# Kernel optimization log

Measured on AMD Instinct MI355X. Metric: run time of the kernel, lower is better.

Reference implementation:

```python
import jax, jax.numpy as jnp
import numpy as np

B, N, D = 4, 2048, 1024
G = 256          # group_size
QK = 128         # query_key_dim
H = 2048         # hidden_dim = int(dim * expansion_factor)
LN_EPS = 1e-5


def setup_inputs() -> dict:
    key = jax.random.key(0)
    ks = jax.random.split(key, 6)
    s = 0.02
    return {
        "x": jax.random.normal(ks[0], (B, N, D), jnp.float32),
        "ln_g": jnp.ones((D,), jnp.float32),
        "ln_b": jnp.zeros((D,), jnp.float32),
        "W_hidden": jax.random.normal(ks[1], (D, 2 * H), jnp.float32) * s,
        "b_hidden": jnp.zeros((2 * H,), jnp.float32),
        "W_qk": jax.random.normal(ks[2], (D, QK), jnp.float32) * s,
        "b_qk": jnp.zeros((QK,), jnp.float32),
        "os_gamma": jnp.ones((4, QK), jnp.float32) + jax.random.normal(ks[3], (4, QK), jnp.float32) * 0.02,
        "os_beta": jnp.zeros((4, QK), jnp.float32),
        "W_out": jax.random.normal(ks[4], (H, D), jnp.float32) * s,
        "b_out": jnp.zeros((D,), jnp.float32),
    }


def _rope(x):
    # x: [b, n, d]; rotary over the sequence dim, matching FLASH.rope(x, dim=1)
    n, d = x.shape[-2], x.shape[-1]
    half = d // 2
    pos = jnp.arange(n, dtype=jnp.float32)
    # freq_seq = -arange(half)/half; inv_freq = 10000 ** (-freq_seq)
    inv_freq = jnp.power(10000.0, jnp.arange(half, dtype=jnp.float32) / half)
    sinusoid = pos[:, None] * inv_freq[None, :]            # [n, half]
    sin, cos = jnp.sin(sinusoid), jnp.cos(sinusoid)
    x1, x2 = jnp.split(x, 2, axis=-1)
    return jnp.concatenate([x1 * cos - x2 * sin, x2 * cos + x1 * sin], axis=-1)


def reference(x, ln_g, ln_b, W_hidden, b_hidden, W_qk, b_qk,
              os_gamma, os_beta, W_out, b_out):
    b, n, d = x.shape
    g = G
    # LayerNorm (biased variance, as torch)
    mu = jnp.mean(x, -1, keepdims=True)
    var = jnp.mean(jnp.square(x - mu), -1, keepdims=True)
    normed = (x - mu) / jnp.sqrt(var + LN_EPS) * ln_g + ln_b

    h = jax.nn.silu(normed @ W_hidden + b_hidden)          # [b, n, 2H]
    v, gate = jnp.split(h, 2, axis=-1)                     # [b, n, H] each
    qk = jax.nn.silu(normed @ W_qk + b_qk)                 # [b, n, QK]

    # OffsetScale: 4 heads -> quad_q, lin_q, quad_k, lin_k
    qk4 = qk[..., None, :] * os_gamma + os_beta            # [b, n, 4, QK]
    quad_q, lin_q, quad_k, lin_k = (_rope(qk4[..., i, :]) for i in range(4))

    pad = (-n) % g
    if pad:
        padf = lambda t: jnp.pad(t, ((0, 0), (0, pad), (0, 0)))
        quad_q, quad_k, lin_q, lin_k, v_p = map(padf, (quad_q, quad_k, lin_q, lin_k, v))
    else:
        v_p = v
    grp = lambda t: t.reshape(b, -1, g, t.shape[-1])       # b (g n) d -> b g n d
    quad_q, quad_k, lin_q, lin_k, vg = map(grp, (quad_q, quad_k, lin_q, lin_k, v_p))

    # group-local quadratic attention with ReLU^2
    sim = jnp.einsum('bgid,bgjd->bgij', quad_q, quad_k) / g
    attn = jnp.square(jax.nn.relu(sim))
    quad_out = jnp.einsum('bgij,bgje->bgie', attn, vg)

    # linear global attention (reduced over groups), divided by full seq len n
    lin_kv = jnp.einsum('bgnd,bgne->bde', lin_k, vg) / n
    lin_out = jnp.einsum('bgnd,bde->bgne', lin_q, lin_kv)

    out = (quad_out + lin_out).reshape(b, -1, vg.shape[-1])[:, :n]
    out = gate * out
    return out @ W_out + b_out + x
```

## Files before the change

kernel.cpp:

```cpp
#include <hip/hip_runtime.h>
#include <stdint.h>

typedef __attribute__((ext_vector_type(8))) short bf16x8_t;
typedef __attribute__((ext_vector_type(4))) float f32x4_t;

#define DI __device__ __forceinline__
#define SBAR() asm volatile("s_barrier" ::: "memory")
#define VMW(n) asm volatile("s_waitcnt vmcnt(" #n ")" ::: "memory")

DI unsigned short f2b(float f) {
  union { float f; unsigned int u; } c; c.f = f;
  unsigned int u = c.u + 0x7FFFu + ((c.u >> 16) & 1u);
  return (unsigned short)(u >> 16);
}
DI unsigned int pack2(float lo, float hi) {
  return (unsigned int)f2b(lo) | ((unsigned int)f2b(hi) << 16);
}
DI float b2f(unsigned short h) {
  union { unsigned int u; float f; } c; c.u = ((unsigned int)h) << 16;
  return c.f;
}
DI float silu_f(float z) { return z / (1.0f + __expf(-z)); }

DI void load_lds16(const unsigned short* g, unsigned short* l) {
  __builtin_amdgcn_global_load_lds(
      (const __attribute__((address_space(1))) unsigned int*)g,
      (__attribute__((address_space(3))) unsigned int*)l,
      16, 0, 0);
}

struct PrepP {
  const float *Wh, *Wo, *Wqk, *x, *g, *b;
  unsigned short *WT, *WoT, *normed;
};

__global__ __launch_bounds__(256) void prep_kernel(PrepP p) {
  const int blk = blockIdx.x;
  const int tx = threadIdx.x & 31, ty = threadIdx.x >> 5;
  if (blk < 6272) {
    const float* in; unsigned short* out; int R, C, gx;
    if (blk < 4096)      { in = p.Wh;  out = p.WT;                 R = 1024; C = 4096; gx = blk; }
    else if (blk < 6144) { in = p.Wo;  out = p.WoT;                R = 2048; C = 1024; gx = blk - 4096; }
    else                 { in = p.Wqk; out = p.WT + 4096 * 1024;   R = 1024; C = 128;  gx = blk - 6144; }
    const int xTiles = C >> 5;
    const int c0 = (gx % xTiles) * 32, r0 = (gx / xTiles) * 32;
    __shared__ float tile[32][33];
#pragma unroll
    for (int i = 0; i < 4; ++i)
      tile[ty + 8 * i][tx] = in[(long)(r0 + ty + 8 * i) * C + c0 + tx];
    __syncthreads();
#pragma unroll
    for (int i = 0; i < 4; ++i)
      out[(long)(c0 + ty + 8 * i) * R + r0 + tx] = f2b(tile[tx][ty + 8 * i]);
  } else {
    const int row = blk - 6272, tid = threadIdx.x;
    __shared__ float red[8];
    float4 v = ((const float4*)(p.x + (long)row * 1024))[tid];
    float s = v.x + v.y + v.z + v.w;
    float ss = v.x * v.x + v.y * v.y + v.z * v.z + v.w * v.w;
    for (int o = 32; o > 0; o >>= 1) { s += __shfl_down(s, o); ss += __shfl_down(ss, o); }
    const int wave = tid >> 6, lane = tid & 63;
    if (lane == 0) { red[wave * 2] = s; red[wave * 2 + 1] = ss; }
    __syncthreads();
    if (tid == 0) {
      float S = red[0] + red[2] + red[4] + red[6];
      float SS = red[1] + red[3] + red[5] + red[7];
      float mu = S * (1.0f / 1024.0f);
      float var = SS * (1.0f / 1024.0f) - mu * mu;
      red[0] = mu; red[1] = rsqrtf(var + 1e-5f);
    }
    __syncthreads();
    const float mu = red[0], rstd = red[1];
    float4 gg = ((const float4*)p.g)[tid];
    float4 bb = ((const float4*)p.b)[tid];
    ushort4 o;
    o.x = f2b((v.x - mu) * rstd * gg.x + bb.x);
    o.y = f2b((v.y - mu) * rstd * gg.y + bb.y);
    o.z = f2b((v.z - mu) * rstd * gg.z + bb.z);
    o.w = f2b((v.w - mu) * rstd * gg.w + bb.w);
    ((ushort4*)(p.normed + (long)row * 1024))[tid] = o;
  }
}

__global__ __launch_bounds__(256) void reduce_cvt(
    const unsigned short* __restrict__ part, unsigned short* __restrict__ out) {
  const int idx = blockIdx.x * 256 + threadIdx.x;
  const int b = idx >> 16, i = idx & 65535;
  float4 s = make_float4(0.f, 0.f, 0.f, 0.f);
#pragma unroll
  for (int sl = 0; sl < 8; ++sl) {
    ushort4 v = ((const ushort4*)part)[(long)(b * 8 + sl) * 65536 + i];
    s.x += b2f(v.x); s.y += b2f(v.y); s.z += b2f(v.z); s.w += b2f(v.w);
  }
  ushort4 o;
  o.x = f2b(s.x); o.y = f2b(s.y); o.z = f2b(s.z); o.w = f2b(s.w);
  ((ushort4*)out)[(long)b * 65536 + i] = o;
}

struct G8P {
  const unsigned short* A;
  const unsigned short* B;
  const float* bias;
  const float* bias2;
  const float* gamma;
  const float* beta;
  unsigned short* vTout;
  unsigned short* gateOut;
  unsigned short* qqO;
  unsigned short* lqO;
  unsigned short* qkhO;
  unsigned short* lkTO;
};

__global__ __launch_bounds__(512, 4) void gemm8p(G8P p) {
  extern __shared__ unsigned char lds[];
  const int tid  = threadIdx.x;
  const int lane = tid & 63;
  const int wave = tid >> 6;
  const bool qk = blockIdx.x < 32;
  int bx, by;
  if (qk) { bx = blockIdx.x; by = 32; }
  else    { const int vg = blockIdx.x - 32; bx = vg >> 5; by = vg & 31; }
  const int wm = (wave & 1) * 128;
  const int wn = (wave >> 1) * 32;
  const int lm = lane & 15;
  const int kb = lane >> 4;

  const int rA  = tid >> 2;
  const int kby = ((tid & 3) << 4) ^ (((rA >> 1) & 3) << 4);
  const unsigned short* gA0 = p.A + (long)(bx * 256 + rA) * 1024 + (kby >> 1);
  const unsigned short* gA1 = gA0 + 128 * 1024;
  const int brow = qk ? 4096 : by * 128;
  const unsigned short* gB0 = p.B + (long)(brow + rA) * 1024 + (kby >> 1);

  const int fxor = (kb << 4) ^ (((lm >> 1) & 3) << 4);

  f32x4_t acc[8][2];
#pragma unroll
  for (int i = 0; i < 8; ++i)
#pragma unroll
    for (int j = 0; j < 2; ++j) acc[i][j] = (f32x4_t){0.f, 0.f, 0.f, 0.f};

  auto stageA = [&](int t) {
    unsigned short* l = (unsigned short*)(lds + (t % 3) * 24576 + wave * 1024);
    load_lds16(gA0 + t * 32, l);
    load_lds16(gA1 + t * 32, (unsigned short*)((unsigned char*)l + 8192));
  };
  auto stageB = [&](int t) {
    unsigned short* l = (unsigned short*)(lds + (t % 3) * 24576 + 16384 + wave * 1024);
    load_lds16(gB0 + t * 32, l);
  };

#pragma unroll
  for (int u = 0; u < 2; ++u) { stageA(u); stageB(u); }
  VMW(3);
  SBAR();

  constexpr int NT = 16;
#pragma unroll 1
  for (int t = 0; t < NT; ++t) {
    const unsigned char* slot = lds + (t % 3) * 24576;
    bf16x8_t bF[2], aF[4];
#pragma unroll
    for (int j = 0; j < 2; ++j)
      bF[j] = *(const bf16x8_t*)(slot + 16384 + (wn + j * 16 + lm) * 64 + fxor);
#pragma unroll
    for (int i = 0; i < 4; ++i)
      aF[i] = *(const bf16x8_t*)(slot + (wm + i * 16 + lm) * 64 + fxor);
    if (t <= NT - 3) stageA(t + 2);
    __builtin_amdgcn_s_setprio(1);
#pragma unroll
    for (int i = 0; i < 4; ++i)
#pragma unroll
      for (int j = 0; j < 2; ++j)
        acc[i][j] = __builtin_amdgcn_mfma_f32_16x16x32_bf16(aF[i], bF[j], acc[i][j], 0, 0, 0);
    __builtin_amdgcn_s_setprio(0);
#pragma unroll
    for (int i = 0; i < 4; ++i)
      aF[i] = *(const bf16x8_t*)(slot + (wm + 64 + i * 16 + lm) * 64 + fxor);
    if (t <= NT - 3) stageB(t + 2);
    __builtin_amdgcn_s_setprio(1);
#pragma unroll
    for (int i = 0; i < 4; ++i)
#pragma unroll
      for (int j = 0; j < 2; ++j)
        acc[i + 4][j] = __builtin_amdgcn_mfma_f32_16x16x32_bf16(aF[i], bF[j], acc[i + 4][j], 0, 0, 0);
    __builtin_amdgcn_s_setprio(0);
    if (t <= NT - 3)      { VMW(3); }
    else if (t == NT - 2) { VMW(0); }
    SBAR();
  }

  if (qk) {
    unsigned short* q16 = (unsigned short*)lds;
#pragma unroll
    for (int i = 0; i < 8; ++i) {
      const int rloc = wm + i * 16 + (lane >> 4) * 4;
#pragma unroll
      for (int j = 0; j < 2; ++j) {
        const int cl = wn + j * 16 + lm;
        const float bb = p.bias2[cl];
#pragma unroll
        for (int r = 0; r < 4; ++r)
          q16[(rloc + r) * 136 + cl] = f2b(silu_f(acc[i][j][r] + bb));
      }
    }
    __syncthreads();
    const int j = tid & 63;
    const int rq = tid >> 6;
    const float freq = powf(10000.0f, (float)j * (1.0f / 64.0f));
    float ga[4], gb[4], ea[4], eb[4];
#pragma unroll
    for (int h = 0; h < 4; ++h) {
      ga[h] = p.gamma[h * 128 + j];  gb[h] = p.gamma[h * 128 + 64 + j];
      ea[h] = p.beta[h * 128 + j];   eb[h] = p.beta[h * 128 + 64 + j];
    }
    unsigned short* outs[3] = {p.qqO, p.lqO, p.qkhO};
    for (int rr = 0; rr < 32; ++rr) {
      const int row = rr * 8 + rq;
      const float x1 = b2f(q16[row * 136 + j]);
      const float x2 = b2f(q16[row * 136 + 64 + j]);
      const int tok = bx * 256 + row;
      const int pos = tok & 2047, bidx = tok >> 11;
      const float ang = (float)pos * freq;
      const float sn = sinf(ang), cs = cosf(ang);
#pragma unroll
      for (int h = 0; h < 3; ++h) {
        const float y1 = x1 * ga[h] + ea[h], y2 = x2 * gb[h] + eb[h];
        outs[h][(long)tok * 128 + j] = f2b(y1 * cs - y2 * sn);
        outs[h][(long)tok * 128 + 64 + j] = f2b(y2 * cs + y1 * sn);
      }
      const float y1 = x1 * ga[3] + ea[3], y2 = x2 * gb[3] + eb[3];
      p.lkTO[((long)bidx * 128 + j) * 2048 + pos] = f2b(y1 * cs - y2 * sn);
      p.lkTO[((long)bidx * 128 + 64 + j) * 2048 + pos] = f2b(y2 * cs + y1 * sn);
    }
  } else if (by < 16) {
    unsigned int* Cx = (unsigned int*)lds;
#pragma unroll
    for (int i = 0; i < 8; ++i) {
      const int c0 = (wm + i * 16) / 2 + (lane >> 4) * 2;
#pragma unroll
      for (int j = 0; j < 2; ++j) {
        const int e = wn + j * 16 + lm;
        const float bb = p.bias[by * 128 + e];
        const float s0 = silu_f(acc[i][j][0] + bb);
        const float s1 = silu_f(acc[i][j][1] + bb);
        const float s2 = silu_f(acc[i][j][2] + bb);
        const float s3 = silu_f(acc[i][j][3] + bb);
        const int x = (e & 7) << 2;
        Cx[e * 128 + (c0 ^ x)]     = pack2(s0, s1);
        Cx[e * 128 + (c0 ^ x) + 1] = pack2(s2, s3);
      }
    }
    __syncthreads();
    const int bq = bx >> 3, nloc0 = (bx & 7) * 256, e0g = by * 128;
    unsigned short* dstBase = p.vTout + ((long)(bq * 2048 + e0g)) * 2048 + nloc0;
#pragma unroll
    for (int rep = 0; rep < 8; ++rep) {
      const int flat = rep * 512 + tid;
      const int e = flat >> 5, q = flat & 31;
      uint4 val = *(const uint4*)(Cx + e * 128 + ((q ^ (e & 7)) << 2));
      *(uint4*)(dstBase + (long)e * 2048 + q * 8) = val;
    }
  } else {
#pragma unroll
    for (int i = 0; i < 8; ++i) {
      const int row0 = bx * 256 + wm + i * 16 + (lane >> 4) * 4;
#pragma unroll
      for (int j = 0; j < 2; ++j) {
        const int colg = (by - 16) * 128 + wn + j * 16 + lm;
        const float bb = p.bias[2048 + colg];
#pragma unroll
        for (int r = 0; r < 4; ++r)
          p.gateOut[(long)(row0 + r) * 2048 + colg] =
              f2b(silu_f(acc[i][j][r] + bb));
      }
    }
  }
}

struct GQLP {
  const unsigned short* attn;
  const unsigned short* vT;
  const unsigned short* lq;
  const unsigned short* lkvT;
  const unsigned short* gateIn;
  unsigned short* outU;
};

__global__ __launch_bounds__(512, 4) void gemmQL(GQLP p) {
  extern __shared__ unsigned char lds[];
  const int tid  = threadIdx.x;
  const int lane = tid & 63;
  const int wave = tid >> 6;
  const int z  = blockIdx.x >> 4;
  const int by = blockIdx.x & 15;
  const int b = z >> 3, g = z & 7;
  const int wm = (wave & 1) * 128;
  const int wn = (wave >> 1) * 32;
  const int lm = lane & 15;
  const int kb = lane >> 4;

  const int rA  = tid >> 2;
  const int kby = ((tid & 3) << 4) ^ (((rA >> 1) & 3) << 4);
  const int swz = kby >> 1;
  const unsigned short* a1 = p.attn + (long)z * 65536 + rA * 256 + swz;
  const unsigned short* a2 = p.lq + ((long)z * 256 + rA) * 128 + swz;
  const unsigned short* b1 = p.vT + (long)b * 4194304 + (long)(by * 128 + rA) * 2048 + g * 256 + swz;
  const unsigned short* b2 = p.lkvT + (long)b * 262144 + (by * 128 + rA) * 128 + swz;
  const int fxor = (kb << 4) ^ (((lm >> 1) & 3) << 4);

  f32x4_t acc[8][2];
#pragma unroll
  for (int i = 0; i < 8; ++i)
#pragma unroll
    for (int j = 0; j < 2; ++j) acc[i][j] = (f32x4_t){0.f, 0.f, 0.f, 0.f};

  auto stageA = [&](int tt) {
    unsigned char* base = lds + (tt % 3) * 24576;
    unsigned short* l  = (unsigned short*)(base + wave * 1024);
    unsigned short* lh = (unsigned short*)(base + wave * 1024 + 8192);
    if (tt < 8) { load_lds16(a1 + tt * 32, l); load_lds16(a1 + 128 * 256 + tt * 32, lh); }
    else { const int k2 = (tt - 8) * 32;
           load_lds16(a2 + k2, l); load_lds16(a2 + 128 * 128 + k2, lh); }
  };
  auto stageB = [&](int tt) {
    unsigned short* l = (unsigned short*)(lds + (tt % 3) * 24576 + 16384 + wave * 1024);
    if (tt < 8) load_lds16(b1 + tt * 32, l);
    else        load_lds16(b2 + (tt - 8) * 32, l);
  };

#pragma unroll
  for (int u = 0; u < 2; ++u) { stageA(u); stageB(u); }
  VMW(3);
  SBAR();

  constexpr int NT = 12;
#pragma unroll 1
  for (int t = 0; t < NT; ++t) {
    const unsigned char* slot = lds + (t % 3) * 24576;
    bf16x8_t bF[2], aF[4];
#pragma unroll
    for (int j = 0; j < 2; ++j)
      bF[j] = *(const bf16x8_t*)(slot + 16384 + (wn + j * 16 + lm) * 64 + fxor);
#pragma unroll
    for (int i = 0; i < 4; ++i)
      aF[i] = *(const bf16x8_t*)(slot + (wm + i * 16 + lm) * 64 + fxor);
    if (t <= NT - 3) stageA(t + 2);
    __builtin_amdgcn_s_setprio(1);
#pragma unroll
    for (int i = 0; i < 4; ++i)
#pragma unroll
      for (int j = 0; j < 2; ++j)
        acc[i][j] = __builtin_amdgcn_mfma_f32_16x16x32_bf16(aF[i], bF[j], acc[i][j], 0, 0, 0);
    __builtin_amdgcn_s_setprio(0);
#pragma unroll
    for (int i = 0; i < 4; ++i)
      aF[i] = *(const bf16x8_t*)(slot + (wm + 64 + i * 16 + lm) * 64 + fxor);
    if (t <= NT - 3) stageB(t + 2);
    __builtin_amdgcn_s_setprio(1);
#pragma unroll
    for (int i = 0; i < 4; ++i)
#pragma unroll
      for (int j = 0; j < 2; ++j)
        acc[i + 4][j] = __builtin_amdgcn_mfma_f32_16x16x32_bf16(aF[i], bF[j], acc[i + 4][j], 0, 0, 0);
    __builtin_amdgcn_s_setprio(0);
    if (t <= NT - 3)      { VMW(3); }
    else if (t == NT - 2) { VMW(0); }
    SBAR();
  }

#pragma unroll
  for (int i = 0; i < 8; ++i) {
    const int row0 = z * 256 + wm + i * 16 + (lane >> 4) * 4;
#pragma unroll
    for (int j = 0; j < 2; ++j) {
      const int col = by * 128 + wn + j * 16 + lm;
#pragma unroll
      for (int r = 0; r < 4; ++r) {
        const long idx = (long)(row0 + r) * 2048 + col;
        p.outU[idx] = f2b(b2f(p.gateIn[idx]) * acc[i][j][r]);
      }
    }
  }
}

struct GWoP {
  const unsigned short* A;
  const unsigned short* B;
  const float* bias;
  const float* xres;
  float* outF;
};

__global__ __launch_bounds__(512, 2) void gemmWo(GWoP p) {
  extern __shared__ unsigned char lds[];
  const int tid  = threadIdx.x;
  const int lane = tid & 63;
  const int wave = tid >> 6;
  const int bx = blockIdx.x >> 3;
  const int by = blockIdx.x & 7;
  const int wm = (wave & 1) * 128;
  const int wn = (wave >> 1) * 32;
  const int lm = lane & 15;
  const int kb = lane >> 4;

  const int rA  = tid >> 2;
  const int kby = ((tid & 3) << 4) ^ (((rA >> 1) & 3) << 4);
  const unsigned short* gA0 = p.A + (long)(bx * 256 + rA) * 2048 + (kby >> 1);
  const unsigned short* gA1 = gA0 + 128 * 2048;
  const unsigned short* gB0 = p.B + (long)(by * 128 + rA) * 2048 + (kby >> 1);
  const int fxor = (kb << 4) ^ (((lm >> 1) & 3) << 4);

  f32x4_t acc[8][2];
#pragma unroll
  for (int i = 0; i < 8; ++i)
#pragma unroll
    for (int j = 0; j < 2; ++j) acc[i][j] = (f32x4_t){0.f, 0.f, 0.f, 0.f};

  auto stageA = [&](int t) {
    unsigned short* l = (unsigned short*)(lds + (t & 3) * 24576 + wave * 1024);
    load_lds16(gA0 + t * 32, l);
    load_lds16(gA1 + t * 32, (unsigned short*)((unsigned char*)l + 8192));
  };
  auto stageB = [&](int t) {
    unsigned short* l = (unsigned short*)(lds + (t & 3) * 24576 + 16384 + wave * 1024);
    load_lds16(gB0 + t * 32, l);
  };

#pragma unroll
  for (int u = 0; u < 3; ++u) { stageA(u); stageB(u); }
  VMW(6);
  SBAR();

  constexpr int NT = 64;
#pragma unroll 1
  for (int t = 0; t < NT; ++t) {
    const unsigned char* slot = lds + (t & 3) * 24576;
    bf16x8_t bF[2], aF[4];
#pragma unroll
    for (int j = 0; j < 2; ++j)
      bF[j] = *(const bf16x8_t*)(slot + 16384 + (wn + j * 16 + lm) * 64 + fxor);
#pragma unroll
    for (int i = 0; i < 4; ++i)
      aF[i] = *(const bf16x8_t*)(slot + (wm + i * 16 + lm) * 64 + fxor);
    if (t <= NT - 4) stageA(t + 3);
    __builtin_amdgcn_s_setprio(1);
#pragma unroll
    for (int i = 0; i < 4; ++i)
#pragma unroll
      for (int j = 0; j < 2; ++j)
        acc[i][j] = __builtin_amdgcn_mfma_f32_16x16x32_bf16(aF[i], bF[j], acc[i][j], 0, 0, 0);
    __builtin_amdgcn_s_setprio(0);
#pragma unroll
    for (int i = 0; i < 4; ++i)
      aF[i] = *(const bf16x8_t*)(slot + (wm + 64 + i * 16 + lm) * 64 + fxor);
    if (t <= NT - 4) stageB(t + 3);
    __builtin_amdgcn_s_setprio(1);
#pragma unroll
    for (int i = 0; i < 4; ++i)
#pragma unroll
      for (int j = 0; j < 2; ++j)
        acc[i + 4][j] = __builtin_amdgcn_mfma_f32_16x16x32_bf16(aF[i], bF[j], acc[i + 4][j], 0, 0, 0);
    __builtin_amdgcn_s_setprio(0);
    if (t <= NT - 4)      { VMW(6); }
    else if (t == NT - 3) { VMW(3); }
    else if (t == NT - 2) { VMW(0); }
    SBAR();
  }

#pragma unroll
  for (int i = 0; i < 8; ++i) {
    const int row0 = bx * 256 + wm + i * 16 + (lane >> 4) * 4;
#pragma unroll
    for (int j = 0; j < 2; ++j) {
      const int col = by * 128 + wn + j * 16 + lm;
      const float bb = p.bias[col];
#pragma unroll
      for (int r = 0; r < 4; ++r) {
        const long idx = (long)(row0 + r) * 1024 + col;
        p.outF[idx] = acc[i][j][r] + bb + p.xres[idx];
      }
    }
  }
}

enum { EPI_ARELU, EPI_PART };

struct GemmP {
  const unsigned short* A;
  const unsigned short* B;
  int K, lda, ldb, ldc, mPerZ;
  long aZ, bZ;
  float scale;
  unsigned short* outU;
};

template <int EPI>
__global__ __launch_bounds__(256, 2) void gemm_bt(GemmP p) {
  __shared__ __align__(16) unsigned char smem[16384];
  unsigned short* As = (unsigned short*)smem;
  unsigned short* Bs = (unsigned short*)(smem + 8192);

  const int tid = threadIdx.x;
  const int lane = tid & 63;
  const int wave = tid >> 6;
  const int bx = blockIdx.x;
  const int by = blockIdx.y;
  const int z = blockIdx.z;

  unsigned short* lA = As + wave * 32 * 32;
  unsigned short* lB = Bs + wave * 32 * 32;
  const int wm = (wave & 1) * 64;
  const int wn = (wave >> 1) * 64;
  const int lm = lane & 15;
  const int kb = lane >> 4;
  const int rowSel = (wave * 32 + (lane >> 2));
  const int colSel = (lane & 3) * 8;

  f32x4_t acc[4][4];
#pragma unroll
  for (int i = 0; i < 4; ++i)
#pragma unroll
    for (int j = 0; j < 4; ++j) acc[i][j] = (f32x4_t){0.f, 0.f, 0.f, 0.f};

  const unsigned short* Ag;
  const unsigned short* Bg;
  if constexpr (EPI == EPI_PART) {
    const int b = z >> 3, s = z & 7;
    Ag = p.A + (long)b * p.aZ + s * 256 + (long)(bx * 128 + rowSel) * p.lda + colSel;
    Bg = p.B + (long)b * p.bZ + s * 256 + (long)(by * 128 + rowSel) * p.ldb + colSel;
  } else {
    Ag = p.A + (long)z * p.aZ + (long)(bx * 128 + rowSel) * p.lda + colSel;
    Bg = p.B + (long)z * p.bZ + (long)(by * 128 + rowSel) * p.ldb + colSel;
  }
  const int a16 = 16 * p.lda, b16 = 16 * p.ldb;
  for (int kt = 0; kt < (p.K >> 5); ++kt) {
    load_lds16(Ag, lA);
    load_lds16(Ag + a16, lA + 512);
    load_lds16(Bg, lB);
    load_lds16(Bg + b16, lB + 512);
    Ag += 32; Bg += 32;
    __syncthreads();
    bf16x8_t aF[4], bF[4];
#pragma unroll
    for (int i = 0; i < 4; ++i)
      aF[i] = *(const bf16x8_t*)(As + (wm + i * 16 + lm) * 32 + kb * 8);
#pragma unroll
    for (int j = 0; j < 4; ++j)
      bF[j] = *(const bf16x8_t*)(Bs + (wn + j * 16 + lm) * 32 + kb * 8);
#pragma unroll
    for (int i = 0; i < 4; ++i)
#pragma unroll
      for (int j = 0; j < 4; ++j)
        acc[i][j] = __builtin_amdgcn_mfma_f32_16x16x32_bf16(aF[i], bF[j], acc[i][j], 0, 0, 0);
    __syncthreads();
  }

#pragma unroll
  for (int i = 0; i < 4; ++i) {
    const int row0 = bx * 128 + wm + i * 16 + (lane >> 4) * 4;
    long rowg0;
    if constexpr (EPI == EPI_PART) rowg0 = row0;
    else rowg0 = (long)z * p.mPerZ + row0;
#pragma unroll
    for (int j = 0; j < 4; ++j) {
      const int col = by * 128 + wn + j * 16 + lm;
      if constexpr (EPI == EPI_ARELU) {
#pragma unroll
        for (int r = 0; r < 4; ++r) {
          float s = acc[i][j][r] * p.scale;
          s = s > 0.f ? s : 0.f;
          p.outU[(rowg0 + r) * (long)p.ldc + col] = f2b(s * s);
        }
      } else {
        unsigned short* slab = p.outU + (long)z * 262144;
#pragma unroll
        for (int r = 0; r < 4; ++r)
          slab[(rowg0 + r) * (long)p.ldc + col] = f2b(acc[i][j][r] * p.scale);
      }
    }
  }
}

extern "C" void kernel_launch(void* const* d_in, const int* in_sizes, int n_in,
                              void* d_out, int out_size, void* d_ws, size_t ws_size,
                              hipStream_t stream) {
  const float* x        = (const float*)d_in[0];
  const float* ln_g     = (const float*)d_in[1];
  const float* ln_b     = (const float*)d_in[2];
  const float* W_hidden = (const float*)d_in[3];
  const float* b_hidden = (const float*)d_in[4];
  const float* W_qk     = (const float*)d_in[5];
  const float* b_qk     = (const float*)d_in[6];
  const float* os_gamma = (const float*)d_in[7];
  const float* os_beta  = (const float*)d_in[8];
  const float* W_out    = (const float*)d_in[9];
  const float* b_out    = (const float*)d_in[10];
  float* out = (float*)d_out;

  char* w = (char*)d_ws;
  auto ws = [&](size_t bytes) { char* p = w; w += bytes; return (unsigned short*)p; };
  unsigned short* WT     = ws(8650752);
  unsigned short* WoT    = ws(4194304);
  unsigned short* normed = ws(16777216);
  unsigned short* vT     = ws(33554432);
  unsigned short* gate   = ws(33554432);
  unsigned short* qq     = ws(2097152);
  unsigned short* qkh    = ws(2097152);
  unsigned short* lq     = ws(2097152);
  unsigned short* lkT    = ws(2097152);
  unsigned short* attn   = ws(4194304);
  unsigned short* lkvP   = ws(16777216);
  unsigned short* lkvT   = ws(2097152);
  unsigned short* A3     = ws(33554432);

  static bool s_attr = false;
  if (!s_attr) {
    hipFuncSetAttribute((const void*)gemm8p,
                        hipFuncAttributeMaxDynamicSharedMemorySize, 73728);
    hipFuncSetAttribute((const void*)gemmQL,
                        hipFuncAttributeMaxDynamicSharedMemorySize, 73728);
    hipFuncSetAttribute((const void*)gemmWo,
                        hipFuncAttributeMaxDynamicSharedMemorySize, 98304);
    s_attr = true;
  }

  {
    PrepP p{W_hidden, W_out, W_qk, x, ln_g, ln_b, WT, WoT, normed};
    prep_kernel<<<14464, 256, 0, stream>>>(p);
  }
  {
    G8P p{normed, WT, b_hidden, b_qk, os_gamma, os_beta,
          vT, gate, qq, lq, qkh, lkT};
    gemm8p<<<dim3(1056, 1, 1), 512, 73728, stream>>>(p);
  }
  {
    GemmP p{}; p.A = qq; p.B = qkh; p.K = 128; p.lda = 128; p.ldb = 128;
    p.ldc = 256; p.mPerZ = 256; p.aZ = 32768; p.bZ = 32768;
    p.scale = 1.f / 256.f; p.outU = attn;
    gemm_bt<EPI_ARELU><<<dim3(2, 2, 32), 256, 0, stream>>>(p);
  }
  {
    GemmP p{}; p.A = vT; p.B = lkT; p.K = 256; p.lda = 2048; p.ldb = 2048;
    p.ldc = 128; p.aZ = 4194304; p.bZ = 262144;
    p.scale = 1.f / 2048.f; p.outU = lkvP;
    gemm_bt<EPI_PART><<<dim3(16, 1, 32), 256, 0, stream>>>(p);
  }
  reduce_cvt<<<1024, 256, 0, stream>>>(lkvP, lkvT);
  {
    GQLP p{attn, vT, lq, lkvT, gate, A3};
    gemmQL<<<dim3(512, 1, 1), 512, 73728, stream>>>(p);
  }
  {
    GWoP p{A3, WoT, b_out, x, out};
    gemmWo<<<dim3(256, 1, 1), 512, 98304, stream>>>(p);
  }
}
```

Before: 297.1 us.

## Shrink output GEMM tile to 128x128 and reuse pipelined kernel for lin_kv partials

The output projection GEMM moves from 256x128 tiles with a 4-stage buffer to 128x128 tiles with a 3-stage buffer and 48KB LDS. That doubles the grid to 512 blocks and allows up to 4 blocks per CU, giving better occupancy and CU coverage. The same templated kernel replaces the simple synchronous gemm_bt for the lin_kv partial products, so that step gets the swizzled, async-pipelined loads. In exchange, the smaller tiles mean more global traffic per FLOP and a shallower prefetch depth.

```diff
diff --git a/kernel.cpp b/kernel.cpp
--- a/kernel.cpp
+++ b/kernel.cpp
@@ -385,66 +385,74 @@
   }
 }
 
-struct GWoP {
+struct G1P {
   const unsigned short* A;
   const unsigned short* B;
   const float* bias;
   const float* xres;
   float* outF;
+  unsigned short* outU;
 };
 
-__global__ __launch_bounds__(512, 2) void gemmWo(GWoP p) {
+template <int EPI>
+__global__ __launch_bounds__(512, 4) void gemm128(G1P p) {
   extern __shared__ unsigned char lds[];
   const int tid  = threadIdx.x;
   const int lane = tid & 63;
   const int wave = tid >> 6;
-  const int bx = blockIdx.x >> 3;
-  const int by = blockIdx.x & 7;
-  const int wm = (wave & 1) * 128;
+  const int wm = (wave & 1) * 64;
   const int wn = (wave >> 1) * 32;
   const int lm = lane & 15;
   const int kb = lane >> 4;
-
   const int rA  = tid >> 2;
   const int kby = ((tid & 3) << 4) ^ (((rA >> 1) & 3) << 4);
-  const unsigned short* gA0 = p.A + (long)(bx * 256 + rA) * 2048 + (kby >> 1);
-  const unsigned short* gA1 = gA0 + 128 * 2048;
-  const unsigned short* gB0 = p.B + (long)(by * 128 + rA) * 2048 + (kby >> 1);
+  const int swz = kby >> 1;
   const int fxor = (kb << 4) ^ (((lm >> 1) & 3) << 4);
 
-  f32x4_t acc[8][2];
-#pragma unroll
-  for (int i = 0; i < 8; ++i)
+  int bx, byz;
+  const unsigned short* gA;
+  const unsigned short* gB;
+  if constexpr (EPI == 0) {
+    bx  = blockIdx.x >> 3;
+    byz = blockIdx.x & 7;
+    gA = p.A + (long)(bx * 128 + rA) * 2048 + swz;
+    gB = p.B + (long)(byz * 128 + rA) * 2048 + swz;
+  } else {
+    byz = blockIdx.x >> 4;
+    bx  = blockIdx.x & 15;
+    const int b = byz >> 3, s = byz & 7;
+    gA = p.A + (long)b * 4194304 + (long)(bx * 128 + rA) * 2048 + s * 256 + swz;
+    gB = p.B + (long)b * 262144 + rA * 2048 + s * 256 + swz;
+  }
+
+  f32x4_t acc[4][2];
+#pragma unroll
+  for (int i = 0; i < 4; ++i)
 #pragma unroll
     for (int j = 0; j < 2; ++j) acc[i][j] = (f32x4_t){0.f, 0.f, 0.f, 0.f};
 
-  auto stageA = [&](int t) {
-    unsigned short* l = (unsigned short*)(lds + (t & 3) * 24576 + wave * 1024);
-    load_lds16(gA0 + t * 32, l);
-    load_lds16(gA1 + t * 32, (unsigned short*)((unsigned char*)l + 8192));
+  auto stage = [&](int t) {
+    unsigned char* base = lds + (t % 3) * 16384;
+    load_lds16(gA + t * 32, (unsigned short*)(base + wave * 1024));
+    load_lds16(gB + t * 32, (unsigned short*)(base + 8192 + wave * 1024));
   };
-  auto stageB = [&](int t) {
-    unsigned short* l = (unsigned short*)(lds + (t & 3) * 24576 + 16384 + wave * 1024);
-    load_lds16(gB0 + t * 32, l);
-  };
-
-#pragma unroll
-  for (int u = 0; u < 3; ++u) { stageA(u); stageB(u); }
-  VMW(6);
+
+  stage(0); stage(1);
+  VMW(2);
   SBAR();
 
-  constexpr int NT = 64;
+  constexpr int NT = (EPI == 0) ? 64 : 8;
 #pragma unroll 1
   for (int t = 0; t < NT; ++t) {
-    const unsigned char* slot = lds + (t & 3) * 24576;
+    const unsigned char* slot = lds + (t % 3) * 16384;
     bf16x8_t bF[2], aF[4];
 #pragma unroll
     for (int j = 0; j < 2; ++j)
-      bF[j] = *(const bf16x8_t*)(slot + 16384 + (wn + j * 16 + lm) * 64 + fxor);
+      bF[j] = *(const bf16x8_t*)(slot + 8192 + (wn + j * 16 + lm) * 64 + fxor);
 #pragma unroll
     for (int i = 0; i < 4; ++i)
       aF[i] = *(const bf16x8_t*)(slot + (wm + i * 16 + lm) * 64 + fxor);
-    if (t <= NT - 4) stageA(t + 3);
+    if (t <= NT - 3) stage(t + 2);
     __builtin_amdgcn_s_setprio(1);
 #pragma unroll
     for (int i = 0; i < 4; ++i)
@@ -452,40 +460,41 @@
       for (int j = 0; j < 2; ++j)
         acc[i][j] = __builtin_amdgcn_mfma_f32_16x16x32_bf16(aF[i], bF[j], acc[i][j], 0, 0, 0);
     __builtin_amdgcn_s_setprio(0);
-#pragma unroll
-    for (int i = 0; i < 4; ++i)
-      aF[i] = *(const bf16x8_t*)(slot + (wm + 64 + i * 16 + lm) * 64 + fxor);
-    if (t <= NT - 4) stageB(t + 3);
-    __builtin_amdgcn_s_setprio(1);
-#pragma unroll
-    for (int i = 0; i < 4; ++i)
-#pragma unroll
-      for (int j = 0; j < 2; ++j)
-        acc[i + 4][j] = __builtin_amdgcn_mfma_f32_16x16x32_bf16(aF[i], bF[j], acc[i + 4][j], 0, 0, 0);
-    __builtin_amdgcn_s_setprio(0);
-    if (t <= NT - 4)      { VMW(6); }
-    else if (t == NT - 3) { VMW(3); }
+    if (t <= NT - 3)      { VMW(2); }
     else if (t == NT - 2) { VMW(0); }
     SBAR();
   }
 
-#pragma unroll
-  for (int i = 0; i < 8; ++i) {
-    const int row0 = bx * 256 + wm + i * 16 + (lane >> 4) * 4;
-#pragma unroll
-    for (int j = 0; j < 2; ++j) {
-      const int col = by * 128 + wn + j * 16 + lm;
-      const float bb = p.bias[col];
-#pragma unroll
-      for (int r = 0; r < 4; ++r) {
-        const long idx = (long)(row0 + r) * 1024 + col;
-        p.outF[idx] = acc[i][j][r] + bb + p.xres[idx];
-      }
-    }
-  }
-}
-
-enum { EPI_ARELU, EPI_PART };
+  if constexpr (EPI == 0) {
+#pragma unroll
+    for (int i = 0; i < 4; ++i) {
+      const int row0 = bx * 128 + wm + i * 16 + (lane >> 4) * 4;
+#pragma unroll
+      for (int j = 0; j < 2; ++j) {
+        const int col = byz * 128 + wn + j * 16 + lm;
+        const float bb = p.bias[col];
+#pragma unroll
+        for (int r = 0; r < 4; ++r) {
+          const long idx = (long)(row0 + r) * 1024 + col;
+          p.outF[idx] = acc[i][j][r] + bb + p.xres[idx];
+        }
+      }
+    }
+  } else {
+    unsigned short* slab = p.outU + (long)byz * 262144;
+#pragma unroll
+    for (int i = 0; i < 4; ++i) {
+      const int row0 = bx * 128 + wm + i * 16 + (lane >> 4) * 4;
+#pragma unroll
+      for (int j = 0; j < 2; ++j) {
+        const int col = wn + j * 16 + lm;
+#pragma unroll
+        for (int r = 0; r < 4; ++r)
+          slab[(row0 + r) * 128 + col] = f2b(acc[i][j][r] * (1.0f / 2048.0f));
+      }
+    }
+  }
+}
 
 struct GemmP {
   const unsigned short* A;
@@ -496,8 +505,7 @@
   unsigned short* outU;
 };
 
-template <int EPI>
-__global__ __launch_bounds__(256, 2) void gemm_bt(GemmP p) {
+__global__ __launch_bounds__(256, 2) void gemm_arelu(GemmP p) {
   __shared__ __align__(16) unsigned char smem[16384];
   unsigned short* As = (unsigned short*)smem;
   unsigned short* Bs = (unsigned short*)(smem + 8192);
@@ -524,16 +532,8 @@
 #pragma unroll
     for (int j = 0; j < 4; ++j) acc[i][j] = (f32x4_t){0.f, 0.f, 0.f, 0.f};
 
-  const unsigned short* Ag;
-  const unsigned short* Bg;
-  if constexpr (EPI == EPI_PART) {
-    const int b = z >> 3, s = z & 7;
-    Ag = p.A + (long)b * p.aZ + s * 256 + (long)(bx * 128 + rowSel) * p.lda + colSel;
-    Bg = p.B + (long)b * p.bZ + s * 256 + (long)(by * 128 + rowSel) * p.ldb + colSel;
-  } else {
-    Ag = p.A + (long)z * p.aZ + (long)(bx * 128 + rowSel) * p.lda + colSel;
-    Bg = p.B + (long)z * p.bZ + (long)(by * 128 + rowSel) * p.ldb + colSel;
-  }
+  const unsigned short* Ag = p.A + (long)z * p.aZ + (long)(bx * 128 + rowSel) * p.lda + colSel;
+  const unsigned short* Bg = p.B + (long)z * p.bZ + (long)(by * 128 + rowSel) * p.ldb + colSel;
   const int a16 = 16 * p.lda, b16 = 16 * p.ldb;
   for (int kt = 0; kt < (p.K >> 5); ++kt) {
     load_lds16(Ag, lA);
@@ -559,25 +559,15 @@
 
 #pragma unroll
   for (int i = 0; i < 4; ++i) {
-    const int row0 = bx * 128 + wm + i * 16 + (lane >> 4) * 4;
-    long rowg0;
-    if constexpr (EPI == EPI_PART) rowg0 = row0;
-    else rowg0 = (long)z * p.mPerZ + row0;
+    const long rowg0 = (long)z * p.mPerZ + bx * 128 + wm + i * 16 + (lane >> 4) * 4;
 #pragma unroll
     for (int j = 0; j < 4; ++j) {
       const int col = by * 128 + wn + j * 16 + lm;
-      if constexpr (EPI == EPI_ARELU) {
-#pragma unroll
-        for (int r = 0; r < 4; ++r) {
-          float s = acc[i][j][r] * p.scale;
-          s = s > 0.f ? s : 0.f;
-          p.outU[(rowg0 + r) * (long)p.ldc + col] = f2b(s * s);
-        }
-      } else {
-        unsigned short* slab = p.outU + (long)z * 262144;
-#pragma unroll
-        for (int r = 0; r < 4; ++r)
-          slab[(rowg0 + r) * (long)p.ldc + col] = f2b(acc[i][j][r] * p.scale);
+#pragma unroll
+      for (int r = 0; r < 4; ++r) {
+        float s = acc[i][j][r] * p.scale;
+        s = s > 0.f ? s : 0.f;
+        p.outU[(rowg0 + r) * (long)p.ldc + col] = f2b(s * s);
       }
     }
   }
@@ -621,8 +611,10 @@
                         hipFuncAttributeMaxDynamicSharedMemorySize, 73728);
     hipFuncSetAttribute((const void*)gemmQL,
                         hipFuncAttributeMaxDynamicSharedMemorySize, 73728);
-    hipFuncSetAttribute((const void*)gemmWo,
-                        hipFuncAttributeMaxDynamicSharedMemorySize, 98304);
+    hipFuncSetAttribute((const void*)gemm128<0>,
+                        hipFuncAttributeMaxDynamicSharedMemorySize, 49152);
+    hipFuncSetAttribute((const void*)gemm128<1>,
+                        hipFuncAttributeMaxDynamicSharedMemorySize, 49152);
     s_attr = true;
   }
 
@@ -639,13 +631,11 @@
     GemmP p{}; p.A = qq; p.B = qkh; p.K = 128; p.lda = 128; p.ldb = 128;
     p.ldc = 256; p.mPerZ = 256; p.aZ = 32768; p.bZ = 32768;
     p.scale = 1.f / 256.f; p.outU = attn;
-    gemm_bt<EPI_ARELU><<<dim3(2, 2, 32), 256, 0, stream>>>(p);
+    gemm_arelu<<<dim3(2, 2, 32), 256, 0, stream>>>(p);
   }
   {
-    GemmP p{}; p.A = vT; p.B = lkT; p.K = 256; p.lda = 2048; p.ldb = 2048;
-    p.ldc = 128; p.aZ = 4194304; p.bZ = 262144;
-    p.scale = 1.f / 2048.f; p.outU = lkvP;
-    gemm_bt<EPI_PART><<<dim3(16, 1, 32), 256, 0, stream>>>(p);
+    G1P p{}; p.A = vT; p.B = lkT; p.outU = lkvP;
+    gemm128<1><<<dim3(512, 1, 1), 512, 49152, stream>>>(p);
   }
   reduce_cvt<<<1024, 256, 0, stream>>>(lkvP, lkvT);
   {
@@ -653,7 +643,7 @@
     gemmQL<<<dim3(512, 1, 1), 512, 73728, stream>>>(p);
   }
   {
-    GWoP p{A3, WoT, b_out, x, out};
-    gemmWo<<<dim3(256, 1, 1), 512, 98304, stream>>>(p);
-  }
-}
+    G1P p{}; p.A = A3; p.B = WoT; p.bias = b_out; p.xres = x; p.outF = out;
+    gemm128<0><<<dim3(512, 1, 1), 512, 49152, stream>>>(p);
+  }
+}
```

Result: slower. 305.0 us (+2.7%).
